# Kernel optimization log

Measured on AMD Instinct MI355X. Metric: run time of the kernel, lower is better.

## Reference

```python
import jax, jax.numpy as jnp
import numpy as np

D_HIDDEN = 512
N_HEADS = 8
D_HEAD = D_HIDDEN // N_HEADS
LAYER_IDX = 0
FACTOR = 0.5 / float(np.sqrt(D_HEAD))


def setup_inputs() -> dict:
    key = jax.random.key(0)
    ks = jax.random.split(key, 16)
    B, N, d = 4, 2048, D_HIDDEN
    s = 1.0 / float(np.sqrt(d))
    inp = {
        "H": jax.random.normal(ks[0], (B, N, d), jnp.float32),
        "V": jax.random.normal(ks[1], (B, N, 3, d), jnp.float32),
        "D": jax.random.normal(ks[2], (B, N, N), jnp.float32),
        "rbf": jax.random.normal(ks[3], (1, B, 1, N, N), jnp.float32),
        "mask": jnp.ones((B, N), jnp.int32),
        # learned parameters (torch nn.Linear: y = x @ W.T + b)
        "Wq": jax.random.normal(ks[4], (4 * d, d), jnp.float32) * s,
        "bq": jax.random.normal(ks[5], (4 * d,), jnp.float32) * s,
        "Wk": jax.random.normal(ks[6], (4 * d, d), jnp.float32) * s,
        "bk": jax.random.normal(ks[7], (4 * d,), jnp.float32) * s,
        "Wv": jax.random.normal(ks[8], (d, d), jnp.float32) * s,
        "bv": jax.random.normal(ks[9], (d,), jnp.float32) * s,
        "Wvv": jax.random.normal(ks[10], (d, d), jnp.float32) * s,
        "Wo": jax.random.normal(ks[11], (d, d), jnp.float32) * s,
        "bo": jax.random.normal(ks[12], (d,), jnp.float32) * s,
        "Wvo": jax.random.normal(ks[13], (d, d), jnp.float32) * s,
    }
    return inp


def reference(H, V, D, rbf, mask, Wq, bq, Wk, bk, Wv, bv, Wvv, Wo, bo, Wvo):
    B, N, d = H.shape
    nh, dh = N_HEADS, D_HEAD
    # projections
    Hq = (H @ Wq.T + bq).reshape(B, N, nh, 4 * dh)
    Hk = (H @ Wk.T + bk).reshape(B, N, nh, 4 * dh)
    Hv = (H @ Wv.T + bv).reshape(B, N, nh, dh)
    # vector values: [B,N,3,nh,dh] -> [B,N,nh,3,dh] -> [B,N,nh,3*dh]
    Vv = (V @ Wvv.T).reshape(B, N, 3, nh, dh)
    Vv = jnp.swapaxes(Vv, -2, -3).reshape(B, N, nh, 3 * dh)
    V_attn = jnp.concatenate([Hv, Vv], axis=-1)  # [B,N,nh,4*dh]
    # additive geometric bias + key mask
    bias = rbf[LAYER_IDX] + D[:, None]  # [B,1,N,N]
    bias = jnp.where(mask[:, None, None, :] == 0, -jnp.inf, bias)
    # attention
    scores = jnp.einsum('bnhd,bmhd->bhnm', Hq, Hk) * FACTOR + bias
    attn = jax.nn.softmax(scores, axis=-1)
    res = jnp.einsum('bhnm,bmhd->bnhd', attn, V_attn)  # [B,N,nh,4*dh]
    # split scalar / vector outputs
    H_res = res[..., :dh].reshape(B, N, d)
    V_res = res[..., dh:].reshape(B, N, nh, 3, dh)
    V_res = jnp.swapaxes(V_res, -2, -3).reshape(B, N, 3, d)
    H_o = H_res @ Wo.T + bo
    V_o = V_res @ Wvo.T
    return H_o, V_o
```

## Files before the change

kernel.cpp:

```cpp
#include <hip/hip_runtime.h>
#include <hip/hip_bf16.h>
#include <stdint.h>

typedef __hip_bfloat16 bf16;
typedef __attribute__((ext_vector_type(8))) short bf16x8;
typedef __attribute__((ext_vector_type(4))) float f32x4;
typedef __attribute__((ext_vector_type(16))) float f32x16;
typedef __attribute__((ext_vector_type(4))) unsigned short u16x4;

#define DEVI __device__ __forceinline__

static constexpr float LOG2E = 1.44269504088896f;
static constexpr float FACTOR_L2E = 0.0625f * 1.44269504088896f;

DEVI unsigned short bfbits(float x) {
  return __builtin_bit_cast(unsigned short, __float2bfloat16(x));
}
DEVI float b2f(unsigned short u) {
  return __builtin_bit_cast(float, (uint32_t)u << 16);
}

__global__ void cvt_plain(const float* __restrict__ src, bf16* __restrict__ dst, int n) {
  int i = (blockIdx.x * 256 + threadIdx.x) * 4;
  if (i >= n) return;
  float4 v = *reinterpret_cast<const float4*>(src + i);
  union { unsigned short u[4]; uint64_t d; } t;
  t.u[0] = bfbits(v.x); t.u[1] = bfbits(v.y); t.u[2] = bfbits(v.z); t.u[3] = bfbits(v.w);
  *reinterpret_cast<uint64_t*>(dst + i) = t.d;
}

__global__ void cvt_vperm(const float* __restrict__ src, bf16* __restrict__ dst) {
  int g = blockIdx.x * 256 + threadIdx.x;
  int k4  = (g & 127) * 4;
  int rem = g >> 7;
  int c  = rem % 3;
  int bn = rem / 3;
  float4 v = *reinterpret_cast<const float4*>(src + (size_t)rem * 512 + k4);
  union { unsigned short u[4]; uint64_t d; } t;
  t.u[0] = bfbits(v.x); t.u[1] = bfbits(v.y); t.u[2] = bfbits(v.z); t.u[3] = bfbits(v.w);
  *reinterpret_cast<uint64_t*>(dst + ((size_t)c * 8192 + bn) * 512 + k4) = t.d;
}

__global__ void cvt_weights(const float* __restrict__ wq, const float* __restrict__ wk,
                            const float* __restrict__ wv, const float* __restrict__ wvv,
                            const float* __restrict__ wo, const float* __restrict__ wvo,
                            bf16* __restrict__ dst) {
  int blk = blockIdx.x;
  const float* s; int off;
  if      (blk < 1024) { s = wq  + blk * 1024;          off = 0       + blk * 1024; }
  else if (blk < 2048) { s = wk  + (blk - 1024) * 1024; off = 1048576 + (blk - 1024) * 1024; }
  else if (blk < 2304) { s = wv  + (blk - 2048) * 1024; off = 2097152 + (blk - 2048) * 1024; }
  else if (blk < 2560) { s = wvv + (blk - 2304) * 1024; off = 2359296 + (blk - 2304) * 1024; }
  else if (blk < 2816) { s = wo  + (blk - 2560) * 1024; off = 2621440 + (blk - 2560) * 1024; }
  else                 { s = wvo + (blk - 2816) * 1024; off = 2883584 + (blk - 2816) * 1024; }
  int i = threadIdx.x * 4;
  float4 v = *reinterpret_cast<const float4*>(s + i);
  union { unsigned short u[4]; uint64_t d; } t;
  t.u[0] = bfbits(v.x); t.u[1] = bfbits(v.y); t.u[2] = bfbits(v.z); t.u[3] = bfbits(v.w);
  *reinterpret_cast<uint64_t*>(dst + off + i) = t.d;
}

__global__ void bias_combine(const float* __restrict__ D, const float* __restrict__ rbf,
                             const int* __restrict__ mask, bf16* __restrict__ Bc) {
  size_t i = ((size_t)blockIdx.x * 256 + threadIdx.x) * 4;
  int col = (int)(i & 2047);
  int b   = (int)(i >> 22);
  float4 d = *reinterpret_cast<const float4*>(D + i);
  float4 r = *reinterpret_cast<const float4*>(rbf + i);
  const int* mrow = mask + b * 2048 + col;
  union { unsigned short u[4]; uint64_t dd; } t;
  t.u[0] = mrow[0] ? bfbits((d.x + r.x) * LOG2E) : bfbits(-1e30f);
  t.u[1] = mrow[1] ? bfbits((d.y + r.y) * LOG2E) : bfbits(-1e30f);
  t.u[2] = mrow[2] ? bfbits((d.z + r.z) * LOG2E) : bfbits(-1e30f);
  t.u[3] = mrow[3] ? bfbits((d.w + r.w) * LOG2E) : bfbits(-1e30f);
  *reinterpret_cast<uint64_t*>(Bc + i) = t.dd;
}

template<int MODE>
__global__ __launch_bounds__(256, 2) void gemm2(const bf16* __restrict__ A,
                                                const bf16* __restrict__ W,
                                                const bf16* __restrict__ W2,
                                                const float* __restrict__ bias,
                                                const float* __restrict__ bias2,
                                                void* __restrict__ outp) {
  constexpr int K = 512;
  __shared__ bf16 As[2][4096];
  __shared__ bf16 Bs[2][4096];
  const int tid = threadIdx.x;
  const int wid = tid >> 6, lane = tid & 63;
  const int lr = lane & 15, lg = lane >> 4;
  const int wr = wid >> 1, wc = wid & 1;
  const int bm = blockIdx.y * 128, bn = blockIdx.x * 128;

  const bf16* Wp;
  if constexpr (MODE == 0) Wp = W;
  else Wp = (blockIdx.y < 64) ? W : W2;

  const int q  = tid >> 2;
  const int ch = ((tid & 3) ^ ((tid >> 3) & 3)) * 8;
  const bf16* Asrc0 = A  + (size_t)(bm + q) * K + ch;
  const bf16* Asrc1 = A  + (size_t)(bm + 64 + q) * K + ch;
  const bf16* Wsrc0 = Wp + (size_t)(bn + q) * K + ch;
  const bf16* Wsrc1 = Wp + (size_t)(bn + 64 + q) * K + ch;
  const int wofs = wid * 1024;

  f32x4 acc[4][4];
#pragma unroll
  for (int m = 0; m < 4; m++)
#pragma unroll
    for (int n = 0; n < 4; n++) acc[m][n] = (f32x4){0.f, 0.f, 0.f, 0.f};

  __builtin_amdgcn_global_load_lds((const char*)Asrc0, (char*)&As[0][0] + wofs,        16, 0, 0);
  __builtin_amdgcn_global_load_lds((const char*)Asrc1, (char*)&As[0][0] + 4096 + wofs, 16, 0, 0);
  __builtin_amdgcn_global_load_lds((const char*)Wsrc0, (char*)&Bs[0][0] + wofs,        16, 0, 0);
  __builtin_amdgcn_global_load_lds((const char*)Wsrc1, (char*)&Bs[0][0] + 4096 + wofs, 16, 0, 0);
  __syncthreads();

  const int fxor = ((lr >> 1) & 3) << 4;
  for (int kt = 0; kt < 16; ++kt) {
    const int cur = kt & 1;
    if (kt < 15) {
      const int nxt = cur ^ 1;
      __builtin_amdgcn_global_load_lds((const char*)(Asrc0 + (kt + 1) * 32), (char*)&As[nxt][0] + wofs,        16, 0, 0);
      __builtin_amdgcn_global_load_lds((const char*)(Asrc1 + (kt + 1) * 32), (char*)&As[nxt][0] + 4096 + wofs, 16, 0, 0);
      __builtin_amdgcn_global_load_lds((const char*)(Wsrc0 + (kt + 1) * 32), (char*)&Bs[nxt][0] + wofs,        16, 0, 0);
      __builtin_amdgcn_global_load_lds((const char*)(Wsrc1 + (kt + 1) * 32), (char*)&Bs[nxt][0] + 4096 + wofs, 16, 0, 0);
    }
    const char* AsC = (const char*)&As[cur][0];
    const char* BsC = (const char*)&Bs[cur][0];
    bf16x8 af[4], bfr[4];
#pragma unroll
    for (int m = 0; m < 4; m++) {
      const int row = wr * 64 + m * 16 + lr;
      af[m] = *reinterpret_cast<const bf16x8*>(AsC + row * 64 + ((lg << 4) ^ fxor));
    }
#pragma unroll
    for (int n = 0; n < 4; n++) {
      const int row = wc * 64 + n * 16 + lr;
      bfr[n] = *reinterpret_cast<const bf16x8*>(BsC + row * 64 + ((lg << 4) ^ fxor));
    }
#pragma unroll
    for (int m = 0; m < 4; m++)
#pragma unroll
      for (int n = 0; n < 4; n++)
        acc[m][n] = __builtin_amdgcn_mfma_f32_16x16x32_bf16(af[m], bfr[n], acc[m][n], 0, 0, 0);
    __syncthreads();
  }

#pragma unroll
  for (int m = 0; m < 4; m++) {
#pragma unroll
    for (int n = 0; n < 4; n++) {
      const int col  = bn + wc * 64 + n * 16 + lr;
      const int row0 = bm + wr * 64 + m * 16 + lg * 4;
      if constexpr (MODE == 0) {
        const int isK = col >> 11;
        const int col2 = col & 2047;
        const float bb = isK ? bias2[col2] : bias[col2];
        const int hh = col2 >> 8, t = col2 & 255;
        bf16* out = (bf16*)outp + (size_t)isK * 16777216;
#pragma unroll
        for (int qq = 0; qq < 4; qq++) {
          const int row = row0 + qq;
          const int b = row >> 11, nn = row & 2047;
          float v = acc[m][n][qq] + bb;
          if (!isK) v *= FACTOR_L2E;
          out[(size_t)((b * 8 + hh) * 2048 + nn) * 256 + t] = __float2bfloat16(v);
        }
      } else if constexpr (MODE == 1) {
        bf16* out = (bf16*)outp;
        const int hh = col >> 6, t = col & 63;
        int dimrow, nn; float bb;
        if (row0 < 8192) {
          const int b = row0 >> 11; nn = row0 & 2047;
          dimrow = (b * 8 + hh) * 256 + t;
          bb = bias[col];
        } else {
          const int r = row0 - 8192;
          const int c = r >> 13, b = (r >> 11) & 3; nn = r & 2047;
          dimrow = (b * 8 + hh) * 256 + 64 + c * 64 + t;
          bb = 0.f;
        }
        const int i4 = (nn >> 2) & 7;
        const int o4 = (i4 & 4) | ((i4 & 1) << 1) | ((i4 >> 1) & 1);
        const int nn2 = (nn & ~31) | (o4 << 2);
        union { unsigned short u[4]; uint64_t d; } pk;
#pragma unroll
        for (int qq = 0; qq < 4; qq++) pk.u[qq] = bfbits(acc[m][n][qq] + bb);
        *reinterpret_cast<uint64_t*>(out + (size_t)dimrow * 2048 + nn2) = pk.d;
      } else {
        float* out = (float*)outp;
        if (row0 < 8192) {
          const float bb = bias[col];
#pragma unroll
          for (int qq = 0; qq < 4; qq++)
            out[(size_t)(row0 + qq) * 512 + col] = acc[m][n][qq] + bb;
        } else {
#pragma unroll
          for (int qq = 0; qq < 4; qq++)
            out[4194304 + (size_t)(row0 - 8192 + qq) * 512 + col] = acc[m][n][qq];
        }
      }
    }
  }
}

__global__ __launch_bounds__(512, 1) void attn_kernel(
    const bf16* __restrict__ Qg, const bf16* __restrict__ Kg, const bf16* __restrict__ Vtg,
    const bf16* __restrict__ Bc, bf16* __restrict__ Hres, bf16* __restrict__ Vres) {
  __shared__ bf16 Ks[3][32 * 256];
  __shared__ bf16 Vs[3][256 * 32];

  const int g = blockIdx.x;
  const int x = g & 7, loc = g >> 3;
  const int bh = x * 4 + (loc & 3);
  const int qt = loc >> 2;
  const int b = bh >> 3, h = bh & 7;
  const int tid = threadIdx.x, w = tid >> 6, lane = tid & 63;
  const int lq = lane & 31, hi = lane >> 5;
  const int q0 = qt * 256 + w * 32;

  const bf16* Qb = Qg + (size_t)bh * 2048 * 256;
  const char* KbC = (const char*)(Kg + (size_t)bh * 2048 * 256);
  const char* VbC = (const char*)(Vtg + (size_t)bh * 256 * 2048);
  const bf16* Bb = Bc + ((size_t)(b * 2048 + q0 + lq)) * 2048 + hi * 4;

  bf16x8 qf[16];
#pragma unroll
  for (int kc = 0; kc < 16; kc++)
    qf[kc] = *reinterpret_cast<const bf16x8*>(Qb + (size_t)(q0 + lq) * 256 + kc * 16 + hi * 8);

  f32x16 O[8];
#pragma unroll
  for (int dt = 0; dt < 8; dt++)
#pragma unroll
    for (int r = 0; r < 16; r++) O[dt][r] = 0.f;
  float mrun = -INFINITY, lrun = 0.f;

  const char* ksrc[2]; const char* vsrc[2];
#pragma unroll
  for (int i = 0; i < 2; i++) {
    const int X = w * 2048 + i * 1024 + lane * 16;
    const int krow = X >> 9, kcol = X & 511;
    ksrc[i] = KbC + (size_t)krow * 512 + (kcol ^ ((krow & 31) << 4));
    const int vrow = X >> 6;
    const int gg = ((vrow >> 1) ^ (vrow >> 3)) & 3;
    vsrc[i] = VbC + (size_t)vrow * 4096 + (((lane & 3) ^ gg) << 4);
  }
  char* ldsKw = (char*)Ks + w * 2048;
  char* ldsVw = (char*)Vs + w * 2048;

  u16x4 bg[4];
#pragma unroll
  for (int i = 0; i < 4; i++) bg[i] = *reinterpret_cast<const u16x4*>(Bb + i * 8);
  __builtin_amdgcn_sched_barrier(0);
#pragma unroll
  for (int i = 0; i < 2; i++) {
    __builtin_amdgcn_global_load_lds(ksrc[i], ldsKw + i * 1024, 16, 0, 0);
    __builtin_amdgcn_global_load_lds(vsrc[i], ldsVw + i * 1024, 16, 0, 0);
  }
  __builtin_amdgcn_sched_barrier(0);
#pragma unroll
  for (int i = 0; i < 2; i++) {
    __builtin_amdgcn_global_load_lds(ksrc[i] + 16384, ldsKw + 16384 + i * 1024, 16, 0, 0);
    __builtin_amdgcn_global_load_lds(vsrc[i] + 64,    ldsVw + 16384 + i * 1024, 16, 0, 0);
  }
  __builtin_amdgcn_sched_barrier(0);
  asm volatile("s_waitcnt vmcnt(4)" ::: "memory");
  __builtin_amdgcn_sched_barrier(0);
  __builtin_amdgcn_s_barrier();

  int c0 = 0;
  int cs = 2;

#pragma unroll 1
  for (int kt = 0; kt < 64; ++kt) {
    const int bt1 = (kt < 63) ? kt + 1 : 63;
    u16x4 bgn[4];
#pragma unroll
    for (int i = 0; i < 4; i++)
      bgn[i] = *reinterpret_cast<const u16x4*>(Bb + bt1 * 32 + i * 8);
    __builtin_amdgcn_sched_barrier(0);
    {
      const int st2 = (kt < 62) ? kt + 2 : 63;
      char* dK = ldsKw + cs * 16384;
      char* dV = ldsVw + cs * 16384;
#pragma unroll
      for (int i = 0; i < 2; i++) {
        __builtin_amdgcn_global_load_lds(ksrc[i] + (size_t)st2 * 16384, dK + i * 1024, 16, 0, 0);
        __builtin_amdgcn_global_load_lds(vsrc[i] + (size_t)st2 * 64,    dV + i * 1024, 16, 0, 0);
      }
    }
    __builtin_amdgcn_sched_barrier(0);

    const char* KsC = (const char*)Ks + c0 * 16384;
    f32x16 s;
#pragma unroll
    for (int r = 0; r < 16; r++) s[r] = 0.f;
    const int kxor = lq << 4;
#pragma unroll
    for (int kc = 0; kc < 16; kc++) {
      bf16x8 kf = *reinterpret_cast<const bf16x8*>(KsC + lq * 512 + ((kc * 32 + hi * 16) ^ kxor));
      s = __builtin_amdgcn_mfma_f32_32x32x16_bf16(kf, qf[kc], s, 0, 0, 0);
    }
#pragma unroll
    for (int r = 0; r < 16; r++)
      s[r] += b2f((unsigned short)bg[r >> 2][r & 3]);

    float m0 = fmaxf(s[0], s[1]),  m1 = fmaxf(s[2], s[3]);
    float m2 = fmaxf(s[4], s[5]),  m3 = fmaxf(s[6], s[7]);
    float m4 = fmaxf(s[8], s[9]),  m5 = fmaxf(s[10], s[11]);
    float m6 = fmaxf(s[12], s[13]), m7 = fmaxf(s[14], s[15]);
    float pmax = fmaxf(fmaxf(fmaxf(m0, m1), fmaxf(m2, m3)),
                       fmaxf(fmaxf(m4, m5), fmaxf(m6, m7)));
    pmax = fmaxf(pmax, __shfl_xor(pmax, 32));

    const bool ok = (pmax <= mrun + 8.f);
    if (!__all((int)ok)) {
      const float mnew = fmaxf(mrun, pmax);
      const float scq = exp2f(mrun - mnew);
      mrun = mnew;
      lrun *= scq;
      float sfac[16];
#pragma unroll
      for (int r = 0; r < 16; r++) sfac[r] = __shfl(scq, (r & 3) + 8 * (r >> 2) + 4 * hi);
#pragma unroll
      for (int dt = 0; dt < 8; dt++)
#pragma unroll
        for (int r = 0; r < 16; r++) O[dt][r] *= sfac[r];
    }

    union { unsigned short u[8]; bf16x8 v; } pa0, pa1;
    float rs = 0.f;
#pragma unroll
    for (int j = 0; j < 8; j++) {
      const float p = exp2f(s[j] - mrun);
      pa0.u[j] = bfbits(p);
      rs += b2f(pa0.u[j]);
    }
#pragma unroll
    for (int j = 0; j < 8; j++) {
      const float p = exp2f(s[8 + j] - mrun);
      pa1.u[j] = bfbits(p);
      rs += b2f(pa1.u[j]);
    }
    rs += __shfl_xor(rs, 32);
    lrun += rs;

    const char* VsC = (const char*)Vs + c0 * 16384;
#pragma unroll
    for (int dt = 0; dt < 8; dt++) {
      const int row = dt * 32 + lq;
      const int gg = ((row >> 1) ^ (row >> 3)) & 3;
      bf16x8 v0 = *reinterpret_cast<const bf16x8*>(VsC + row * 64 + ((hi ^ gg) << 4));
      bf16x8 v1 = *reinterpret_cast<const bf16x8*>(VsC + row * 64 + (((2 + hi) ^ gg) << 4));
      O[dt] = __builtin_amdgcn_mfma_f32_32x32x16_bf16(pa0.v, v0, O[dt], 0, 0, 0);
      O[dt] = __builtin_amdgcn_mfma_f32_32x32x16_bf16(pa1.v, v1, O[dt], 0, 0, 0);
    }

    asm volatile("s_waitcnt vmcnt(5)" ::: "memory");
    __builtin_amdgcn_sched_barrier(0);
    __builtin_amdgcn_s_barrier();

    c0 = (c0 == 2) ? 0 : c0 + 1;
    cs = (cs == 2) ? 0 : cs + 1;
#pragma unroll
    for (int i = 0; i < 4; i++) bg[i] = bgn[i];
  }

  const float rli = 1.0f / lrun;
  float rl[16];
#pragma unroll
  for (int r = 0; r < 16; r++) rl[r] = __shfl(rli, (r & 3) + 8 * (r >> 2) + 4 * hi);
#pragma unroll
  for (int dt = 0; dt < 8; dt++) {
    const int d = dt * 32 + lq;
#pragma unroll
    for (int r = 0; r < 16; r++) {
      const int row = q0 + (r & 3) + 8 * (r >> 2) + 4 * hi;
      const float v = O[dt][r] * rl[r];
      if (d < 64) {
        Hres[(size_t)(b * 2048 + row) * 512 + h * 64 + d] = __float2bfloat16(v);
      } else {
        const int c = (d - 64) >> 6, t = (d - 64) & 63;
        Vres[((size_t)(b * 2048 + row) * 3 + c) * 512 + h * 64 + t] = __float2bfloat16(v);
      }
    }
  }
}

extern "C" void kernel_launch(void* const* d_in, const int* in_sizes, int n_in,
                              void* d_out, int out_size, void* d_ws, size_t ws_size,
                              hipStream_t stream) {
  const float* H   = (const float*)d_in[0];
  const float* V   = (const float*)d_in[1];
  const float* Dm  = (const float*)d_in[2];
  const float* rbf = (const float*)d_in[3];
  const int*   mask= (const int*)d_in[4];
  const float* Wq  = (const float*)d_in[5];
  const float* bq  = (const float*)d_in[6];
  const float* Wk  = (const float*)d_in[7];
  const float* bk  = (const float*)d_in[8];
  const float* Wv  = (const float*)d_in[9];
  const float* bv  = (const float*)d_in[10];
  const float* Wvv = (const float*)d_in[11];
  const float* Wo  = (const float*)d_in[12];
  const float* bo  = (const float*)d_in[13];
  const float* Wvo = (const float*)d_in[14];

  char* ws = (char*)d_ws;
  bf16* Hbf  = (bf16*)(ws);
  bf16* Wall = (bf16*)(ws + 33554432);
  bf16* Qw   = (bf16*)(ws + 39845888);
  bf16* Kw   = Qw + 16777216;
  bf16* Vtw  = (bf16*)(ws + 106954752);
  bf16* Hres = Hbf;
  bf16* Wqb  = Wall;
  bf16* Wvb  = Wall + 2097152;
  bf16* Wvvb = Wall + 2359296;
  bf16* Wob  = Wall + 2621440;
  bf16* Wvob = Wall + 2883584;
  bf16* Bcb  = (bf16*)d_out;

  bias_combine<<<16384, 256, 0, stream>>>(Dm, rbf, mask, Bcb);
  cvt_plain<<<4096, 256, 0, stream>>>(H, Hbf, 4194304);
  cvt_vperm<<<12288, 256, 0, stream>>>(V, Hbf + 4194304);
  cvt_weights<<<3072, 256, 0, stream>>>(Wq, Wk, Wv, Wvv, Wo, Wvo, Wall);

  gemm2<0><<<dim3(32, 64), 256, 0, stream>>>(Hbf, Wqb, nullptr, bq, bk, Qw);
  gemm2<1><<<dim3(4, 256), 256, 0, stream>>>(Hbf, Wvb, Wvvb, bv, nullptr, Vtw);

  attn_kernel<<<256, 512, 0, stream>>>(Qw, Kw, Vtw, Bcb, Hres, Hbf + 4194304);

  gemm2<2><<<dim3(4, 256), 256, 0, stream>>>(Hbf, Wob, Wvob, bo, nullptr, d_out);
}
```

Before: 451.7 us.

## Process two KV tiles per iteration with double-buffered LDS and halved barriers

The attention main loop now handles two 32-key tiles per iteration. K and V are double-buffered across four LDS slots instead of a three-slot ring, and loads are issued one iteration ahead. This halves the number of block barriers and waitcnts and drops the ring-index bookkeeping. In exchange it uses more LDS, waits with vmcnt(0) instead of partial counts, and loads the bias for both tiles at once, which raises register pressure and may expose load latency.

```diff
diff --git a/kernel.cpp b/kernel.cpp
--- a/kernel.cpp
+++ b/kernel.cpp
@@ -208,8 +208,8 @@
 __global__ __launch_bounds__(512, 1) void attn_kernel(
     const bf16* __restrict__ Qg, const bf16* __restrict__ Kg, const bf16* __restrict__ Vtg,
     const bf16* __restrict__ Bc, bf16* __restrict__ Hres, bf16* __restrict__ Vres) {
-  __shared__ bf16 Ks[3][32 * 256];
-  __shared__ bf16 Vs[3][256 * 32];
+  __shared__ bf16 Ks[4][32 * 256];
+  __shared__ bf16 Vs[4][256 * 32];
 
   const int g = blockIdx.x;
   const int x = g & 7, loc = g >> 3;
@@ -247,125 +247,188 @@
     const int gg = ((vrow >> 1) ^ (vrow >> 3)) & 3;
     vsrc[i] = VbC + (size_t)vrow * 4096 + (((lane & 3) ^ gg) << 4);
   }
-  char* ldsKw = (char*)Ks + w * 2048;
-  char* ldsVw = (char*)Vs + w * 2048;
-
-  u16x4 bg[4];
-#pragma unroll
-  for (int i = 0; i < 4; i++) bg[i] = *reinterpret_cast<const u16x4*>(Bb + i * 8);
+  char* ldsK = (char*)Ks + w * 2048;
+  char* ldsV = (char*)Vs + w * 2048;
+
+  u16x4 bg[8];
+#pragma unroll
+  for (int i = 0; i < 4; i++) {
+    bg[i]     = *reinterpret_cast<const u16x4*>(Bb + i * 8);
+    bg[4 + i] = *reinterpret_cast<const u16x4*>(Bb + 32 + i * 8);
+  }
   __builtin_amdgcn_sched_barrier(0);
 #pragma unroll
-  for (int i = 0; i < 2; i++) {
-    __builtin_amdgcn_global_load_lds(ksrc[i], ldsKw + i * 1024, 16, 0, 0);
-    __builtin_amdgcn_global_load_lds(vsrc[i], ldsVw + i * 1024, 16, 0, 0);
+  for (int hh = 0; hh < 2; hh++) {
+#pragma unroll
+    for (int i = 0; i < 2; i++) {
+      __builtin_amdgcn_global_load_lds(ksrc[i] + (size_t)hh * 16384, ldsK + hh * 16384 + i * 1024, 16, 0, 0);
+      __builtin_amdgcn_global_load_lds(vsrc[i] + (size_t)hh * 64,    ldsV + hh * 16384 + i * 1024, 16, 0, 0);
+    }
   }
   __builtin_amdgcn_sched_barrier(0);
-#pragma unroll
-  for (int i = 0; i < 2; i++) {
-    __builtin_amdgcn_global_load_lds(ksrc[i] + 16384, ldsKw + 16384 + i * 1024, 16, 0, 0);
-    __builtin_amdgcn_global_load_lds(vsrc[i] + 64,    ldsVw + 16384 + i * 1024, 16, 0, 0);
-  }
-  __builtin_amdgcn_sched_barrier(0);
-  asm volatile("s_waitcnt vmcnt(4)" ::: "memory");
+  asm volatile("s_waitcnt vmcnt(0)" ::: "memory");
   __builtin_amdgcn_sched_barrier(0);
   __builtin_amdgcn_s_barrier();
 
-  int c0 = 0;
-  int cs = 2;
-
 #pragma unroll 1
-  for (int kt = 0; kt < 64; ++kt) {
-    const int bt1 = (kt < 63) ? kt + 1 : 63;
-    u16x4 bgn[4];
-#pragma unroll
-    for (int i = 0; i < 4; i++)
-      bgn[i] = *reinterpret_cast<const u16x4*>(Bb + bt1 * 32 + i * 8);
+  for (int kt = 0; kt < 32; ++kt) {
+    const int buf = kt & 1;
+    const int nb = (buf ^ 1) * 2;
+    const int tn = (kt < 31) ? 2 * kt + 2 : 62;
+
+#pragma unroll
+    for (int hh = 0; hh < 2; hh++) {
+#pragma unroll
+      for (int i = 0; i < 2; i++) {
+        __builtin_amdgcn_global_load_lds(ksrc[i] + (size_t)(tn + hh) * 16384, ldsK + (nb + hh) * 16384 + i * 1024, 16, 0, 0);
+        __builtin_amdgcn_global_load_lds(vsrc[i] + (size_t)(tn + hh) * 64,    ldsV + (nb + hh) * 16384 + i * 1024, 16, 0, 0);
+      }
+    }
     __builtin_amdgcn_sched_barrier(0);
+
     {
-      const int st2 = (kt < 62) ? kt + 2 : 63;
-      char* dK = ldsKw + cs * 16384;
-      char* dV = ldsVw + cs * 16384;
-#pragma unroll
-      for (int i = 0; i < 2; i++) {
-        __builtin_amdgcn_global_load_lds(ksrc[i] + (size_t)st2 * 16384, dK + i * 1024, 16, 0, 0);
-        __builtin_amdgcn_global_load_lds(vsrc[i] + (size_t)st2 * 64,    dV + i * 1024, 16, 0, 0);
-      }
-    }
-    __builtin_amdgcn_sched_barrier(0);
-
-    const char* KsC = (const char*)Ks + c0 * 16384;
-    f32x16 s;
-#pragma unroll
-    for (int r = 0; r < 16; r++) s[r] = 0.f;
-    const int kxor = lq << 4;
-#pragma unroll
-    for (int kc = 0; kc < 16; kc++) {
-      bf16x8 kf = *reinterpret_cast<const bf16x8*>(KsC + lq * 512 + ((kc * 32 + hi * 16) ^ kxor));
-      s = __builtin_amdgcn_mfma_f32_32x32x16_bf16(kf, qf[kc], s, 0, 0, 0);
-    }
-#pragma unroll
-    for (int r = 0; r < 16; r++)
-      s[r] += b2f((unsigned short)bg[r >> 2][r & 3]);
-
-    float m0 = fmaxf(s[0], s[1]),  m1 = fmaxf(s[2], s[3]);
-    float m2 = fmaxf(s[4], s[5]),  m3 = fmaxf(s[6], s[7]);
-    float m4 = fmaxf(s[8], s[9]),  m5 = fmaxf(s[10], s[11]);
-    float m6 = fmaxf(s[12], s[13]), m7 = fmaxf(s[14], s[15]);
-    float pmax = fmaxf(fmaxf(fmaxf(m0, m1), fmaxf(m2, m3)),
-                       fmaxf(fmaxf(m4, m5), fmaxf(m6, m7)));
-    pmax = fmaxf(pmax, __shfl_xor(pmax, 32));
-
-    const bool ok = (pmax <= mrun + 8.f);
-    if (!__all((int)ok)) {
-      const float mnew = fmaxf(mrun, pmax);
-      const float scq = exp2f(mrun - mnew);
-      mrun = mnew;
-      lrun *= scq;
-      float sfac[16];
-#pragma unroll
-      for (int r = 0; r < 16; r++) sfac[r] = __shfl(scq, (r & 3) + 8 * (r >> 2) + 4 * hi);
-#pragma unroll
-      for (int dt = 0; dt < 8; dt++)
-#pragma unroll
-        for (int r = 0; r < 16; r++) O[dt][r] *= sfac[r];
-    }
-
-    union { unsigned short u[8]; bf16x8 v; } pa0, pa1;
-    float rs = 0.f;
-#pragma unroll
-    for (int j = 0; j < 8; j++) {
-      const float p = exp2f(s[j] - mrun);
-      pa0.u[j] = bfbits(p);
-      rs += b2f(pa0.u[j]);
-    }
-#pragma unroll
-    for (int j = 0; j < 8; j++) {
-      const float p = exp2f(s[8 + j] - mrun);
-      pa1.u[j] = bfbits(p);
-      rs += b2f(pa1.u[j]);
-    }
-    rs += __shfl_xor(rs, 32);
-    lrun += rs;
-
-    const char* VsC = (const char*)Vs + c0 * 16384;
-#pragma unroll
-    for (int dt = 0; dt < 8; dt++) {
-      const int row = dt * 32 + lq;
-      const int gg = ((row >> 1) ^ (row >> 3)) & 3;
-      bf16x8 v0 = *reinterpret_cast<const bf16x8*>(VsC + row * 64 + ((hi ^ gg) << 4));
-      bf16x8 v1 = *reinterpret_cast<const bf16x8*>(VsC + row * 64 + (((2 + hi) ^ gg) << 4));
-      O[dt] = __builtin_amdgcn_mfma_f32_32x32x16_bf16(pa0.v, v0, O[dt], 0, 0, 0);
-      O[dt] = __builtin_amdgcn_mfma_f32_32x32x16_bf16(pa1.v, v1, O[dt], 0, 0, 0);
-    }
-
-    asm volatile("s_waitcnt vmcnt(5)" ::: "memory");
+      const char* KsC = (const char*)Ks + (buf * 2 + 0) * 16384;
+      const char* VsC = (const char*)Vs + (buf * 2 + 0) * 16384;
+      f32x16 s;
+#pragma unroll
+      for (int r = 0; r < 16; r++) s[r] = 0.f;
+      const int kxor = lq << 4;
+#pragma unroll
+      for (int kc = 0; kc < 16; kc++) {
+        bf16x8 kf = *reinterpret_cast<const bf16x8*>(KsC + lq * 512 + ((kc * 32 + hi * 16) ^ kxor));
+        s = __builtin_amdgcn_mfma_f32_32x32x16_bf16(kf, qf[kc], s, 0, 0, 0);
+      }
+#pragma unroll
+      for (int r = 0; r < 16; r++)
+        s[r] += b2f((unsigned short)bg[r >> 2][r & 3]);
+
+      float m0 = fmaxf(s[0], s[1]),  m1 = fmaxf(s[2], s[3]);
+      float m2 = fmaxf(s[4], s[5]),  m3 = fmaxf(s[6], s[7]);
+      float m4 = fmaxf(s[8], s[9]),  m5 = fmaxf(s[10], s[11]);
+      float m6 = fmaxf(s[12], s[13]), m7 = fmaxf(s[14], s[15]);
+      float pmax = fmaxf(fmaxf(fmaxf(m0, m1), fmaxf(m2, m3)),
+                         fmaxf(fmaxf(m4, m5), fmaxf(m6, m7)));
+      pmax = fmaxf(pmax, __shfl_xor(pmax, 32));
+
+      const bool ok = (pmax <= mrun + 8.f);
+      if (!__all((int)ok)) {
+        const float mnew = fmaxf(mrun, pmax);
+        const float scq = exp2f(mrun - mnew);
+        mrun = mnew;
+        lrun *= scq;
+        float sfac[16];
+#pragma unroll
+        for (int r = 0; r < 16; r++) sfac[r] = __shfl(scq, (r & 3) + 8 * (r >> 2) + 4 * hi);
+#pragma unroll
+        for (int dt = 0; dt < 8; dt++)
+#pragma unroll
+          for (int r = 0; r < 16; r++) O[dt][r] *= sfac[r];
+      }
+
+      union { unsigned short u[8]; bf16x8 v; } pa0, pa1;
+      float rs = 0.f;
+#pragma unroll
+      for (int j = 0; j < 8; j++) {
+        const float p = exp2f(s[j] - mrun);
+        pa0.u[j] = bfbits(p);
+        rs += b2f(pa0.u[j]);
+      }
+#pragma unroll
+      for (int j = 0; j < 8; j++) {
+        const float p = exp2f(s[8 + j] - mrun);
+        pa1.u[j] = bfbits(p);
+        rs += b2f(pa1.u[j]);
+      }
+      rs += __shfl_xor(rs, 32);
+      lrun += rs;
+
+#pragma unroll
+      for (int dt = 0; dt < 8; dt++) {
+        const int row = dt * 32 + lq;
+        const int gg = ((row >> 1) ^ (row >> 3)) & 3;
+        bf16x8 v0 = *reinterpret_cast<const bf16x8*>(VsC + row * 64 + ((hi ^ gg) << 4));
+        bf16x8 v1 = *reinterpret_cast<const bf16x8*>(VsC + row * 64 + (((2 + hi) ^ gg) << 4));
+        O[dt] = __builtin_amdgcn_mfma_f32_32x32x16_bf16(pa0.v, v0, O[dt], 0, 0, 0);
+        O[dt] = __builtin_amdgcn_mfma_f32_32x32x16_bf16(pa1.v, v1, O[dt], 0, 0, 0);
+      }
+    }
+
+    {
+      const char* KsC = (const char*)Ks + (buf * 2 + 1) * 16384;
+      const char* VsC = (const char*)Vs + (buf * 2 + 1) * 16384;
+      f32x16 s;
+#pragma unroll
+      for (int r = 0; r < 16; r++) s[r] = 0.f;
+      const int kxor = lq << 4;
+#pragma unroll
+      for (int kc = 0; kc < 16; kc++) {
+        bf16x8 kf = *reinterpret_cast<const bf16x8*>(KsC + lq * 512 + ((kc * 32 + hi * 16) ^ kxor));
+        s = __builtin_amdgcn_mfma_f32_32x32x16_bf16(kf, qf[kc], s, 0, 0, 0);
+      }
+#pragma unroll
+      for (int r = 0; r < 16; r++)
+        s[r] += b2f((unsigned short)bg[4 + (r >> 2)][r & 3]);
+
+#pragma unroll
+      for (int i = 0; i < 4; i++) {
+        bg[i]     = *reinterpret_cast<const u16x4*>(Bb + (size_t)tn * 32 + i * 8);
+        bg[4 + i] = *reinterpret_cast<const u16x4*>(Bb + (size_t)(tn + 1) * 32 + i * 8);
+      }
+
+      float m0 = fmaxf(s[0], s[1]),  m1 = fmaxf(s[2], s[3]);
+      float m2 = fmaxf(s[4], s[5]),  m3 = fmaxf(s[6], s[7]);
+      float m4 = fmaxf(s[8], s[9]),  m5 = fmaxf(s[10], s[11]);
+      float m6 = fmaxf(s[12], s[13]), m7 = fmaxf(s[14], s[15]);
+      float pmax = fmaxf(fmaxf(fmaxf(m0, m1), fmaxf(m2, m3)),
+                         fmaxf(fmaxf(m4, m5), fmaxf(m6, m7)));
+      pmax = fmaxf(pmax, __shfl_xor(pmax, 32));
+
+      const bool ok = (pmax <= mrun + 8.f);
+      if (!__all((int)ok)) {
+        const float mnew = fmaxf(mrun, pmax);
+        const float scq = exp2f(mrun - mnew);
+        mrun = mnew;
+        lrun *= scq;
+        float sfac[16];
+#pragma unroll
+        for (int r = 0; r < 16; r++) sfac[r] = __shfl(scq, (r & 3) + 8 * (r >> 2) + 4 * hi);
+#pragma unroll
+        for (int dt = 0; dt < 8; dt++)
+#pragma unroll
+          for (int r = 0; r < 16; r++) O[dt][r] *= sfac[r];
+      }
+
+      union { unsigned short u[8]; bf16x8 v; } pa0, pa1;
+      float rs = 0.f;
+#pragma unroll
+      for (int j = 0; j < 8; j++) {
+        const float p = exp2f(s[j] - mrun);
+        pa0.u[j] = bfbits(p);
+        rs += b2f(pa0.u[j]);
+      }
+#pragma unroll
+      for (int j = 0; j < 8; j++) {
+        const float p = exp2f(s[8 + j] - mrun);
+        pa1.u[j] = bfbits(p);
+        rs += b2f(pa1.u[j]);
+      }
+      rs += __shfl_xor(rs, 32);
+      lrun += rs;
+
+#pragma unroll
+      for (int dt = 0; dt < 8; dt++) {
+        const int row = dt * 32 + lq;
+        const int gg = ((row >> 1) ^ (row >> 3)) & 3;
+        bf16x8 v0 = *reinterpret_cast<const bf16x8*>(VsC + row * 64 + ((hi ^ gg) << 4));
+        bf16x8 v1 = *reinterpret_cast<const bf16x8*>(VsC + row * 64 + (((2 + hi) ^ gg) << 4));
+        O[dt] = __builtin_amdgcn_mfma_f32_32x32x16_bf16(pa0.v, v0, O[dt], 0, 0, 0);
+        O[dt] = __builtin_amdgcn_mfma_f32_32x32x16_bf16(pa1.v, v1, O[dt], 0, 0, 0);
+      }
+    }
+
+    asm volatile("s_waitcnt vmcnt(0)" ::: "memory");
     __builtin_amdgcn_sched_barrier(0);
     __builtin_amdgcn_s_barrier();
-
-    c0 = (c0 == 2) ? 0 : c0 + 1;
-    cs = (cs == 2) ? 0 : cs + 1;
-#pragma unroll
-    for (int i = 0; i < 4; i++) bg[i] = bgn[i];
   }
 
   const float rli = 1.0f / lrun;
```

Measured after the change: 485.0 us. 1.07x slower.
